# Kernel optimization log

Measured on AMD Instinct MI355X. Metric: run time of the kernel, lower is better.

The kernel has to match this reference:

```python
import jax, jax.numpy as jnp
import numpy as np

V, E, H, B, S, T = 32000, 512, 1024, 32, 64, 64

def setup_inputs() -> dict:
    key = jax.random.key(0)
    ks = jax.random.split(key, 26)
    p = 0.02  # param init scale
    inp = {
        "enc_h": jax.random.normal(ks[0], (B, S, 2 * H), dtype=jnp.float32),
        "prev_s": jax.random.normal(ks[1], (B, H), dtype=jnp.float32),
        "target": jax.random.randint(ks[2], (B, T), 0, V, dtype=jnp.int32),
        "embed": jax.random.normal(ks[3], (V, E), dtype=jnp.float32) * p,
        # Attention params
        "att_Wenc": jax.random.normal(ks[4], (2 * H, H), dtype=jnp.float32) * p,
        "att_benc": jnp.zeros((H,), dtype=jnp.float32),
        "att_Wprev": jax.random.normal(ks[5], (H, H), dtype=jnp.float32) * p,
        "att_bprev": jnp.zeros((H,), dtype=jnp.float32),
        "att_wlin": jax.random.normal(ks[6], (H, 1), dtype=jnp.float32) * p,
        "att_blin": jnp.zeros((1,), dtype=jnp.float32),
        # DecoderCell gate params (input/hidden/ctx -> 2H)
        "dc_Wi": jax.random.normal(ks[7], (E, 2 * H), dtype=jnp.float32) * p,
        "dc_bi": jnp.zeros((2 * H,), dtype=jnp.float32),
        "dc_Wh": jax.random.normal(ks[8], (H, 2 * H), dtype=jnp.float32) * p,
        "dc_bh": jnp.zeros((2 * H,), dtype=jnp.float32),
        "dc_Wc": jax.random.normal(ks[9], (2 * H, 2 * H), dtype=jnp.float32) * p,
        "dc_bc": jnp.zeros((2 * H,), dtype=jnp.float32),
        # DecoderCell candidate params (-> H)
        "dc_Wi2": jax.random.normal(ks[10], (E, H), dtype=jnp.float32) * p,
        "dc_bi2": jnp.zeros((H,), dtype=jnp.float32),
        "dc_Wh2": jax.random.normal(ks[11], (H, H), dtype=jnp.float32) * p,
        "dc_bh2": jnp.zeros((H,), dtype=jnp.float32),
        "dc_Wc2": jax.random.normal(ks[12], (2 * H, H), dtype=jnp.float32) * p,
        "dc_bc2": jnp.zeros((H,), dtype=jnp.float32),
        # dec2word
        "out_W": jax.random.normal(ks[13], (H, V), dtype=jnp.float32) * p,
        "out_b": jnp.zeros((V,), dtype=jnp.float32),
    }
    return inp


def reference(enc_h, prev_s, target, embed, att_Wenc, att_benc, att_Wprev,
              att_bprev, att_wlin, att_blin, dc_Wi, dc_bi, dc_Wh, dc_bh,
              dc_Wc, dc_bc, dc_Wi2, dc_bi2, dc_Wh2, dc_bh2, dc_Wc2, dc_bc2,
              out_W, out_b):
    h = prev_s.shape[-1]
    # Precompute attention key projection (weights fixed across timesteps)
    enc_proj = enc_h @ att_Wenc + att_benc          # B x S x H
    xs = jnp.transpose(embed[target], (1, 0, 2))    # T x B x E

    def step(s_prev, x_t):
        # Bahdanau attention
        q = s_prev @ att_Wprev + att_bprev                       # B x H
        score = jnp.tanh(enc_proj + q[:, None, :]) @ att_wlin + att_blin  # B x S x 1
        alpha = jax.nn.softmax(score[..., 0], axis=1)            # B x S (over seq)
        ctx = jnp.einsum('bs,bsh->bh', alpha, enc_h)             # B x 2H
        # GRU-like cell (original uses only the first chunk of gates)
        gates = (x_t @ dc_Wi + dc_bi) + (s_prev @ dc_Wh + dc_bh) + (ctx @ dc_Wc + dc_bc)
        reset = jax.nn.sigmoid(gates[:, :h])
        s_tilde = jnp.tanh((x_t @ dc_Wi2 + dc_bi2) + (s_prev @ dc_Wh2 + dc_bh2) + (ctx @ dc_Wc2 + dc_bc2))
        s_new = (1.0 - reset) * s_prev + reset * s_tilde
        return s_new, s_new

    final_s, dec_h = jax.lax.scan(step, prev_s, xs)   # dec_h: T x B x H
    outputs = jnp.transpose(dec_h, (1, 0, 2)) @ out_W + out_b  # B x T x V
    return outputs, final_s
```

## Files before the change

kernel.cpp:

```cpp
#include <hip/hip_runtime.h>

#define B_   32
#define S_   64
#define T_   64
#define H_   1024
#define H2_  2048
#define E_   512
#define V_   32000
#define K3_  3072
#define BT_  2048

typedef unsigned short u16;
typedef __attribute__((ext_vector_type(8))) short short8_t;
typedef __attribute__((ext_vector_type(4))) float f32x4;

__device__ __forceinline__ u16 f2bf(float f) {
  unsigned x = __float_as_uint(f);
  unsigned r = (x + 0x7fffu + ((x >> 16) & 1u)) >> 16;
  return (u16)r;
}
__device__ __forceinline__ float bf2f(u16 h) {
  return __uint_as_float(((unsigned)h) << 16);
}
__device__ __forceinline__ float frcp(float x) { return __builtin_amdgcn_rcpf(x); }
__device__ __forceinline__ float ftanh(float x) {
  float e = __expf(2.f * x);
  return 1.f - 2.f * frcp(e + 1.f);
}
__device__ __forceinline__ float fsigm(float x) {
  return frcp(1.f + __expf(-x));
}

#define KEEPV(x) asm volatile("" : "+v"(x))

__device__ __forceinline__ void st_u16(u16* p, u16 v) {
  __hip_atomic_store(p, v, __ATOMIC_RELAXED, __HIP_MEMORY_SCOPE_AGENT);
}
__device__ __forceinline__ void st_f32(float* p, float v) {
  __hip_atomic_store(p, v, __ATOMIC_RELAXED, __HIP_MEMORY_SCOPE_AGENT);
}

#define MB_ (1ull << 20)
#define KB_ (1ull << 10)
#define X_OFF    (0)
#define XGR_OFF  (4*MB_)
#define XG2_OFF  (12*MB_)
#define ENCT_OFF (20*MB_)
#define QFV_OFF  (20*MB_)
#define WQF_OFF  (28*MB_)
#define WGF_OFF  (30*MB_)
#define XSV_OFF  (28*MB_)
#define XCV_OFF  (36*MB_)
#define WOT_OFF  (0)
#define DECH_OFF (54*MB_)
#define XS0_OFF  (58*MB_)
#define BAS_OFF  (58*MB_ + 128*KB_)
#define BCR_OFF  (58*MB_ + 132*KB_)
#define BC2_OFF  (58*MB_ + 136*KB_)
#define WLB_OFF  (58*MB_ + 140*KB_)
#define BAR_OFF  (58*MB_ + 144*KB_)

__device__ __forceinline__ u16* xs_hi(char* w, int t) {
  return (u16*)(t == 0 ? (w + XS0_OFF) : (w + XSV_OFF + (size_t)(t - 1) * 131072));
}
__device__ __forceinline__ u16* xc_hi(char* w, int t) {
  return (u16*)(w + XCV_OFF + (size_t)t * 262144);
}
__device__ __forceinline__ float* qf_v(char* w, int t) {
  return (float*)(w + QFV_OFF + (size_t)t * 131072);
}


__global__ void k_gather(float* __restrict__ x, const float* __restrict__ embed,
                         const int* __restrict__ tgt) {
  int bid = blockIdx.x;
  int t = bid >> 5, b = bid & 31;
  int row = tgt[b * T_ + t];
  const float4* src = (const float4*)(embed + (size_t)row * E_);
  float4* dst = (float4*)(x + (size_t)bid * E_);
  dst[threadIdx.x] = src[threadIdx.x];
}

__global__ void k_biascomb(float* bcr, float* bc2o, float* bas, u16* wlb,
                           const float* bi, const float* bh, const float* bc,
                           const float* bi2, const float* bh2, const float* bc2i,
                           const float* benc, const float* bprev, const float* wlin) {
  int j = blockIdx.x * 256 + threadIdx.x;
  if (j < H_) {
    bcr[j]  = bi[j]  + bh[j]  + bc[j];
    bc2o[j] = bi2[j] + bh2[j] + bc2i[j];
    bas[j]  = benc[j] + bprev[j];
    wlb[j]  = f2bf(wlin[j]);
  }
}

__global__ __launch_bounds__(256) void k_gemm(
    const float* __restrict__ A, int lda,
    const float* __restrict__ Bm, int ldb,
    void* __restrict__ Cv, int ldc, int outBf16,
    const float* __restrict__ bias,
    int mtiles, int ntiles, int K) {
  __shared__ u16 As[128][72];
  __shared__ u16 Bs[128][72];
  int nwg = mtiles * ntiles;
  int bid = blockIdx.x;
  int cpx = nwg >> 3;
  int lb = (bid & 7) * cpx + (bid >> 3);
  int ntb = lb / mtiles, mtb = lb - ntb * mtiles;
  size_t m0 = (size_t)mtb * 128, n0 = (size_t)ntb * 128;
  int t = threadIdx.x, lane = t & 63, wid = t >> 6;
  int wr = (wid >> 1) * 64, wc = (wid & 1) * 64;
  f32x4 acc[4][4] = {};
  for (int k0 = 0; k0 < K; k0 += 64) {
    #pragma unroll
    for (int i = 0; i < 8; ++i) {
      int f4 = i * 256 + t;
      int row = f4 >> 4, c4 = (f4 & 15) << 2;
      float4 v = *(const float4*)(A + (m0 + row) * (size_t)lda + k0 + c4);
      ushort4 u; u.x = f2bf(v.x); u.y = f2bf(v.y); u.z = f2bf(v.z); u.w = f2bf(v.w);
      *(ushort4*)&As[row][c4] = u;
    }
    #pragma unroll
    for (int i = 0; i < 8; ++i) {
      int f4 = i * 256 + t;
      int kr = f4 >> 5, c4 = (f4 & 31) << 2;
      float4 v = *(const float4*)(Bm + (size_t)(k0 + kr) * ldb + n0 + c4);
      Bs[c4 + 0][kr] = f2bf(v.x);
      Bs[c4 + 1][kr] = f2bf(v.y);
      Bs[c4 + 2][kr] = f2bf(v.z);
      Bs[c4 + 3][kr] = f2bf(v.w);
    }
    __syncthreads();
    #pragma unroll
    for (int kk = 0; kk < 64; kk += 32) {
      int ko = kk + (lane >> 4) * 8;
      short8_t am[4], bn[4];
      #pragma unroll
      for (int m = 0; m < 4; ++m) am[m] = *(const short8_t*)&As[wr + m * 16 + (lane & 15)][ko];
      #pragma unroll
      for (int n = 0; n < 4; ++n) bn[n] = *(const short8_t*)&Bs[wc + n * 16 + (lane & 15)][ko];
      #pragma unroll
      for (int m = 0; m < 4; ++m)
        #pragma unroll
        for (int n = 0; n < 4; ++n)
          acc[m][n] = __builtin_amdgcn_mfma_f32_16x16x32_bf16(am[m], bn[n], acc[m][n], 0, 0, 0);
    }
    __syncthreads();
  }
  #pragma unroll
  for (int n = 0; n < 4; ++n) {
    int col = wc + n * 16 + (lane & 15);
    float bv = bias ? bias[n0 + col] : 0.f;
    #pragma unroll
    for (int m = 0; m < 4; ++m) {
      size_t row = m0 + wr + m * 16 + ((lane >> 4) << 2);
      #pragma unroll
      for (int r = 0; r < 4; ++r) {
        float val = acc[m][n][r] + bv;
        if (outBf16) ((u16*)Cv)[(row + r) * (size_t)ldc + n0 + col] = f2bf(val);
        else ((float*)Cv)[(row + r) * (size_t)ldc + n0 + col] = val;
      }
    }
  }
}

__global__ __launch_bounds__(256) void k_transE(u16* __restrict__ encT,
                                                const float* __restrict__ enc_h) {
  __shared__ u16 ld[64][68];
  int b = blockIdx.x >> 5, et = blockIdx.x & 31;
  int e0 = et * 64;
  int t = threadIdx.x;
  #pragma unroll
  for (int i = 0; i < 4; ++i) {
    int f4 = i * 256 + t;
    int si = f4 >> 4, e4 = (f4 & 15) << 2;
    float4 v = *(const float4*)(enc_h + ((size_t)(b * 64 + si)) * H2_ + e0 + e4);
    ld[si][e4 + 0] = f2bf(v.x); ld[si][e4 + 1] = f2bf(v.y);
    ld[si][e4 + 2] = f2bf(v.z); ld[si][e4 + 3] = f2bf(v.w);
  }
  __syncthreads();
  #pragma unroll
  for (int i = 0; i < 2; ++i) {
    int idx = i * 256 + t;
    int e = idx >> 3, s8 = (idx & 7) << 3;
    short8_t o;
    #pragma unroll
    for (int k = 0; k < 8; ++k) o[k] = (short)ld[s8 + k][e];
    *(short8_t*)(encT + ((size_t)(e0 + e)) * 2048 + b * 64 + s8) = o;
  }
}

__global__ __launch_bounds__(256) void k_packq(u16* __restrict__ wqf,
                                               const float* __restrict__ W) {
  __shared__ float ld[64][33];
  int jt = blockIdx.x & 31, kt = blockIdx.x >> 5;
  int c0 = jt * 32, k0 = kt * 64;
  int t = threadIdx.x;
  #pragma unroll
  for (int i = 0; i < 8; ++i) {
    int idx = i * 256 + t; int kr = idx >> 5, jc = idx & 31;
    ld[kr][jc] = W[(size_t)(k0 + kr) * H_ + c0 + jc];
  }
  __syncthreads();
  int u = t;
  int gl = u >> 7, kbl = (u >> 6) & 1, sub = (u >> 4) & 3, c = u & 15;
  int colLoc = gl * 16 + c;
  int gG = jt * 2 + gl, KB = kt * 2 + kbl;
  size_t lin = ((size_t)(gG * 32 + KB) * 4 + sub) * 16 + c;
  short8_t o;
  #pragma unroll
  for (int j = 0; j < 8; ++j) o[j] = (short)f2bf(ld[kbl * 32 + sub * 8 + j][colLoc]);
  *(short8_t*)(wqf + lin * 8) = o;
}

__global__ __launch_bounds__(256) void k_packg(
    u16* __restrict__ wgf, const float* __restrict__ Wh, const float* __restrict__ Wc,
    const float* __restrict__ Wh2, const float* __restrict__ Wc2) {
  __shared__ float ld[64][33];
  int sel = blockIdx.x & 1;
  int jt  = (blockIdx.x >> 1) & 31;
  int kt  = blockIdx.x >> 6;
  int k0 = kt * 64, j0 = jt * 32;
  int t = threadIdx.x;
  const float* srcW = (k0 < H_) ? (sel ? Wh2 : Wh) : (sel ? Wc2 : Wc);
  int ldw = sel ? H_ : H2_;
  int koff = (k0 < H_) ? k0 : (k0 - H_);
  #pragma unroll
  for (int i = 0; i < 8; ++i) {
    int idx = i * 256 + t; int kr = idx >> 5, jc = idx & 31;
    ld[kr][jc] = srcW[(size_t)(koff + kr) * ldw + j0 + jc];
  }
  __syncthreads();
  #pragma unroll
  for (int it = 0; it < 2; ++it) {
    int u = it * 256 + t;
    int m = u & 3, sub = (u >> 2) & 3, kbl = (u >> 4) & 1, islo = (u >> 5) & 1, gg = u >> 6;
    int jjLoc = gg * 4 + m;
    int p = 2 * (j0 + jjLoc) + sel;
    int g = p >> 3, cc = p & 7;
    int c = cc + 8 * islo;
    int KB = kt * 2 + kbl;
    size_t lin = ((size_t)(g * 96 + KB) * 4 + sub) * 16 + c;
    short8_t o;
    #pragma unroll
    for (int j = 0; j < 8; ++j) {
      float v = ld[kbl * 32 + sub * 8 + j][jjLoc];
      u16 h = f2bf(v);
      o[j] = (short)(islo ? f2bf(v - bf2f(h)) : h);
    }
    *(short8_t*)(wgf + lin * 8) = o;
  }
}

__global__ __launch_bounds__(256) void k_wtrans(u16* __restrict__ wot,
                                                const float* __restrict__ W, int nbase) {
  __shared__ u16 ld[64][68];
  int nt = blockIdx.x % 250, kt = blockIdx.x / 250;
  int n0 = nbase + nt * 64, k0 = kt * 64;
  int t = threadIdx.x;
  #pragma unroll
  for (int i = 0; i < 4; ++i) {
    int f4 = i * 256 + t;
    int kr = f4 >> 4, n4 = (f4 & 15) << 2;
    float4 v = *(const float4*)(W + (size_t)(k0 + kr) * V_ + n0 + n4);
    ld[kr][n4 + 0] = f2bf(v.x); ld[kr][n4 + 1] = f2bf(v.y);
    ld[kr][n4 + 2] = f2bf(v.z); ld[kr][n4 + 3] = f2bf(v.w);
  }
  __syncthreads();
  #pragma unroll
  for (int i = 0; i < 2; ++i) {
    int idx = i * 256 + t;
    int n = idx >> 3, k8 = (idx & 7) << 3;
    short8_t o;
    #pragma unroll
    for (int k = 0; k < 8; ++k) o[k] = (short)ld[k8 + k][n];
    *(short8_t*)(wot + ((size_t)(nt * 64 + n)) * H_ + k0 + k8) = o;
  }
}

__global__ __launch_bounds__(256) void k_gemm2(
    const u16* __restrict__ A, const u16* __restrict__ Bt,
    float* __restrict__ C, const float* __restrict__ bias, int n0g) {
  __shared__ u16 As[128][72];
  __shared__ u16 Bs[128][72];
  int bid = blockIdx.x;
  int lb = (bid & 7) * 250 + (bid >> 3);
  int mtb = lb & 15, ntb = lb >> 4;
  size_t m0 = (size_t)mtb * 128;
  size_t nl0 = (size_t)ntb * 128;
  int t = threadIdx.x, lane = t & 63, wid = t >> 6;
  int wr = (wid >> 1) * 64, wc = (wid & 1) * 64;
  f32x4 acc[4][4] = {};
  for (int k0 = 0; k0 < H_; k0 += 64) {
    #pragma unroll
    for (int i = 0; i < 4; ++i) {
      int idx = i * 256 + t;
      int row = idx >> 3, c8 = (idx & 7) << 3;
      *(short8_t*)&As[row][c8] = *(const short8_t*)(A + (m0 + row) * H_ + k0 + c8);
      *(short8_t*)&Bs[row][c8] = *(const short8_t*)(Bt + (nl0 + row) * H_ + k0 + c8);
    }
    __syncthreads();
    #pragma unroll
    for (int kk = 0; kk < 64; kk += 32) {
      int ko = kk + (lane >> 4) * 8;
      short8_t am[4], bn[4];
      #pragma unroll
      for (int m = 0; m < 4; ++m) am[m] = *(const short8_t*)&As[wr + m * 16 + (lane & 15)][ko];
      #pragma unroll
      for (int n = 0; n < 4; ++n) bn[n] = *(const short8_t*)&Bs[wc + n * 16 + (lane & 15)][ko];
      #pragma unroll
      for (int m = 0; m < 4; ++m)
        #pragma unroll
        for (int n = 0; n < 4; ++n)
          acc[m][n] = __builtin_amdgcn_mfma_f32_16x16x32_bf16(am[m], bn[n], acc[m][n], 0, 0, 0);
    }
    __syncthreads();
  }
  #pragma unroll
  for (int n = 0; n < 4; ++n) {
    int col = n0g + (int)nl0 + wc + n * 16 + (lane & 15);
    float bv = bias[col];
    #pragma unroll
    for (int m = 0; m < 4; ++m) {
      size_t row = m0 + wr + m * 16 + ((lane >> 4) << 2);
      #pragma unroll
      for (int r = 0; r < 4; ++r)
        C[(row + r) * (size_t)V_ + col] = acc[m][n][r] + bv;
    }
  }
}


__device__ __forceinline__ void gridbar(int* bar, int target) {
  asm volatile("s_waitcnt vmcnt(0)" ::: "memory");
  __syncthreads();
  if (threadIdx.x == 0) {
    int* leafcnt = bar;
    int* root    = bar + 512;
    int* leafep  = bar + 768;
    int li = blockIdx.x >> 3;
    if (__hip_atomic_fetch_add(&leafcnt[li * 16], 1, __ATOMIC_RELAXED, __HIP_MEMORY_SCOPE_AGENT) == 7) {
      __hip_atomic_store(&leafcnt[li * 16], 0, __ATOMIC_RELAXED, __HIP_MEMORY_SCOPE_AGENT);
      if (__hip_atomic_fetch_add(root, 1, __ATOMIC_RELAXED, __HIP_MEMORY_SCOPE_AGENT) == 31) {
        __hip_atomic_store(root, 0, __ATOMIC_RELAXED, __HIP_MEMORY_SCOPE_AGENT);
        #pragma unroll
        for (int i = 0; i < 32; ++i)
          __hip_atomic_store(&leafep[i * 16], target, __ATOMIC_RELAXED, __HIP_MEMORY_SCOPE_AGENT);
      }
    }
    while (__hip_atomic_load(&leafep[li * 16], __ATOMIC_RELAXED, __HIP_MEMORY_SCOPE_AGENT) != target)
      __builtin_amdgcn_s_sleep(2);
  }
  __syncthreads();
}

#define MFMA16(a, b, c) __builtin_amdgcn_mfma_f32_16x16x32_bf16((a), (b), (c), 0, 0, 0)

__global__ __launch_bounds__(512, 1) void k_mega(
    char* w, u16* __restrict__ dech, float* __restrict__ fout,
    const u16* __restrict__ wqf, const u16* __restrict__ wgf,
    const u16* __restrict__ encp, const u16* __restrict__ encT,
    const float* __restrict__ xgr, const float* __restrict__ xg2,
    const float* __restrict__ prev_s, const u16* __restrict__ wlb,
    int* bar) {
  const int t = threadIdx.x, blk = blockIdx.x;
  const int lane = t & 63, wid = t >> 6;
  const int l15 = lane & 15, l4 = lane >> 4;
  const int klo = l4 * 8;
  __shared__ short8_t wg_lds[6144];
  __shared__ f32x4 scr[1024];
  __shared__ float sc[64];
  int ep = 0;

  for (int i = t; i < 6144; i += 512)
    wg_lds[i] = *(const short8_t*)(wgf + ((size_t)blk * 6144 + i) * 8);

  const int gq = blk & 63;
  short8_t wq[4];
  #pragma unroll
  for (int i = 0; i < 4; ++i) {
    wq[i] = *(const short8_t*)(wqf + ((size_t)(gq * 32 + wid * 4 + i) * 64 + lane) * 8);
    KEEPV(wq[i]);
  }
  const int bb = blk >> 3, eg = blk & 7;
  short8_t epv[8][2];
  #pragma unroll
  for (int r = 0; r < 8; ++r) {
    const u16* p = encp + ((size_t)(bb * 64 + wid * 8 + r)) * H_ + lane * 16;
    epv[r][0] = *(const short8_t*)(p);     KEEPV(epv[r][0]);
    epv[r][1] = *(const short8_t*)(p + 8); KEEPV(epv[r][1]);
  }
  short8_t wlv[2];
  wlv[0] = *(const short8_t*)(wlb + lane * 16);     KEEPV(wlv[0]);
  wlv[1] = *(const short8_t*)(wlb + lane * 16 + 8); KEEPV(wlv[1]);
  const int eloc = t >> 1, half = t & 1;
  const int ecol = eg * 256 + eloc;
  short8_t et[4];
  #pragma unroll
  for (int i = 0; i < 4; ++i) {
    et[i] = *(const short8_t*)(encT + (size_t)ecol * 2048 + bb * 64 + half * 32 + i * 8);
    KEEPV(et[i]);
  }

  const int pc4 = blk * 8 + l15, jcol = pc4 >> 1, isc = pc4 & 1;
  const int rb = wid * 16 + l4 * 4;
  const bool fin = (wid < 2) && (l15 < 8);
  float sreg[4] = {0.f, 0.f, 0.f, 0.f};

  {
    int idx = blk * 512 + t;
    u16* xs0h = xs_hi(w, 0);
    u16* xs0l = xs0h + B_ * H_;
    if (idx < B_ * H_) {
      float v = prev_s[idx];
      u16 h = f2bf(v);
      st_u16(&xs0h[idx], h);
      st_u16(&xs0l[idx], f2bf(v - bf2f(h)));
    }
    if (fin) {
      #pragma unroll
      for (int r = 0; r < 4; ++r) sreg[r] = prev_s[(rb + r) * H_ + jcol];
    }
  }
  gridbar(bar, ++ep);

  for (int ts = 0; ts < T_; ++ts) {
    const u16* xsh = xs_hi(w, ts);
    const u16* xsl = xsh + B_ * H_;
    u16* xch = xc_hi(w, ts);
    u16* xcl = xch + B_ * H2_;
    float* qfv = qf_v(w, ts);

    float xv[4] = {0.f, 0.f, 0.f, 0.f};
    if (fin) {
      const float* xg = isc ? xg2 : xgr;
      #pragma unroll
      for (int r = 0; r < 4; ++r)
        xv[r] = xg[((size_t)ts * B_ + rb + r) * H_ + jcol];
    }
    short8_t pA[4], pB[4];
    #pragma unroll
    for (int i = 0; i < 4; ++i) {
      int k = (wid + 8 * i) * 32 + klo;
      pA[i] = *(const short8_t*)(xsh + l15 * H_ + k);        KEEPV(pA[i]);
      pB[i] = *(const short8_t*)(xsh + (l15 + 16) * H_ + k); KEEPV(pB[i]);
    }

    if (blk < 64) {
      f32x4 aA = {}, aB = {};
      #pragma unroll
      for (int i = 0; i < 4; ++i) {
        int kof = (wid * 4 + i) * 32 + klo;
        short8_t avA = *(const short8_t*)(xsh + l15 * H_ + kof);
        short8_t avB = *(const short8_t*)(xsh + (l15 + 16) * H_ + kof);
        aA = MFMA16(avA, wq[i], aA);
        aB = MFMA16(avB, wq[i], aB);
      }
      scr[(wid * 2 + 0) * 64 + lane] = aA;
      scr[(wid * 2 + 1) * 64 + lane] = aB;
      __syncthreads();
      if (wid < 2) {
        f32x4 s = scr[wid * 64 + lane];
        #pragma unroll
        for (int i = 1; i < 8; ++i) s += scr[(i * 2 + wid) * 64 + lane];
        int col = gq * 16 + l15;
        #pragma unroll
        for (int r = 0; r < 4; ++r)
          st_f32(&qfv[(size_t)(rb + r) * H_ + col], s[r]);
      }
    }
    gridbar(bar, ++ep);

    {
      float qv[16];
      #pragma unroll
      for (int i = 0; i < 4; ++i) {
        float4 s0 = *(const float4*)(qfv + (size_t)bb * H_ + lane * 16 + i * 4);
        qv[i * 4 + 0] = s0.x; qv[i * 4 + 1] = s0.y;
        qv[i * 4 + 2] = s0.z; qv[i * 4 + 3] = s0.w;
      }
      #pragma unroll
      for (int r = 0; r < 8; ++r) {
        float p = 0.f;
        #pragma unroll
        for (int jj = 0; jj < 16; ++jj)
          p += ftanh(bf2f((u16)epv[r][jj >> 3][jj & 7]) + qv[jj]) * bf2f((u16)wlv[jj >> 3][jj & 7]);
        #pragma unroll
        for (int off = 32; off; off >>= 1) p += __shfl_xor(p, off, 64);
        if (lane == 0) sc[wid * 8 + r] = p;
      }
      __syncthreads();
      if (wid == 0) {
        float v = sc[lane];
        float m = v;
        #pragma unroll
        for (int off = 32; off; off >>= 1) m = fmaxf(m, __shfl_xor(m, off, 64));
        float e = __expf(v - m);
        float s = e;
        #pragma unroll
        for (int off = 32; off; off >>= 1) s += __shfl_xor(s, off, 64);
        sc[lane] = e * frcp(s);
      }
      __syncthreads();
      {
        float a = 0.f;
        #pragma unroll
        for (int i = 0; i < 4; ++i)
          #pragma unroll
          for (int j = 0; j < 8; ++j)
            a += sc[half * 32 + i * 8 + j] * bf2f((u16)et[i][j]);
        a += __shfl_xor(a, 1, 64);
        if (half == 0) {
          u16 hh = f2bf(a);
          st_u16(&xch[bb * H2_ + ecol], hh);
          st_u16(&xcl[bb * H2_ + ecol], f2bf(a - bf2f(hh)));
        }
      }
    }
    gridbar(bar, ++ep);

    {
      f32x4 aA = {}, aB = {};
      short8_t loA[4], loB[4];
      #pragma unroll
      for (int i = 0; i < 4; ++i) {
        int k = (wid + 8 * i) * 32 + klo;
        loA[i] = *(const short8_t*)(xsl + l15 * H_ + k);
        loB[i] = *(const short8_t*)(xsl + (l15 + 16) * H_ + k);
      }
      #pragma unroll
      for (int i = 0; i < 4; ++i) {
        short8_t bv = wg_lds[(wid + 8 * i) * 64 + lane];
        aA = MFMA16(pA[i], bv, aA);
        aB = MFMA16(pB[i], bv, aB);
      }
      #pragma unroll
      for (int i = 0; i < 4; ++i) {
        short8_t bv = wg_lds[(wid + 8 * i) * 64 + lane];
        aA = MFMA16(loA[i], bv, aA);
        aB = MFMA16(loB[i], bv, aB);
      }
      #pragma unroll
      for (int i = 4; i < 12; ++i) {
        int kb = wid + 8 * i;
        int k = kb * 32 + klo - H_;
        short8_t hA = *(const short8_t*)(xch + l15 * H2_ + k);
        short8_t lA = *(const short8_t*)(xcl + l15 * H2_ + k);
        short8_t hB = *(const short8_t*)(xch + (l15 + 16) * H2_ + k);
        short8_t lB = *(const short8_t*)(xcl + (l15 + 16) * H2_ + k);
        short8_t bv = wg_lds[kb * 64 + lane];
        aA = MFMA16(hA, bv, aA);
        aA = MFMA16(lA, bv, aA);
        aB = MFMA16(hB, bv, aB);
        aB = MFMA16(lB, bv, aB);
      }
      scr[(wid * 2 + 0) * 64 + lane] = aA;
      scr[(wid * 2 + 1) * 64 + lane] = aB;
      __syncthreads();
      if (wid < 2) {
        f32x4 s = scr[wid * 64 + lane];
        #pragma unroll
        for (int i = 1; i < 8; ++i) s += scr[(i * 2 + wid) * 64 + lane];
        float tot[4];
        #pragma unroll
        for (int r = 0; r < 4; ++r) tot[r] = s[r] + __shfl_xor(s[r], 8, 64);
        if (l15 < 8) {
          u16* nsh = xs_hi(w, ts + 1);
          u16* nsl = nsh + B_ * H_;
          #pragma unroll
          for (int r = 0; r < 4; ++r) {
            int brow = rb + r;
            float pre = tot[r] + xv[r];
            float mate = __shfl_xor(pre, 1, 64);
            float rpre = isc ? mate : pre;
            float cpre = isc ? pre : mate;
            float rg = fsigm(rpre);
            float cg = ftanh(cpre);
            float sp = sreg[r];
            float sn = sp + rg * (cg - sp);
            sreg[r] = sn;
            if (!isc) {
              u16 hh = f2bf(sn);
              st_u16(&nsh[brow * H_ + jcol], hh);
              st_u16(&nsl[brow * H_ + jcol], f2bf(sn - bf2f(hh)));
              dech[((size_t)brow * T_ + ts) * H_ + jcol] = hh;
              if (ts == T_ - 1) fout[brow * H_ + jcol] = sn;
            }
          }
        }
      }
    }
    gridbar(bar, ++ep);
  }
}


extern "C" void kernel_launch(void* const* d_in, const int* in_sizes, int n_in,
                              void* d_out, int out_size, void* d_ws, size_t ws_size,
                              hipStream_t stream) {
  const float* enc_h    = (const float*)d_in[0];
  const float* prev_s   = (const float*)d_in[1];
  const int*   target   = (const int*)d_in[2];
  const float* embed    = (const float*)d_in[3];
  const float* att_Wenc = (const float*)d_in[4];
  const float* att_benc = (const float*)d_in[5];
  const float* att_Wprev= (const float*)d_in[6];
  const float* att_bprev= (const float*)d_in[7];
  const float* att_wlin = (const float*)d_in[8];
  const float* dc_Wi    = (const float*)d_in[10];
  const float* dc_bi    = (const float*)d_in[11];
  const float* dc_Wh    = (const float*)d_in[12];
  const float* dc_bh    = (const float*)d_in[13];
  const float* dc_Wc    = (const float*)d_in[14];
  const float* dc_bc    = (const float*)d_in[15];
  const float* dc_Wi2   = (const float*)d_in[16];
  const float* dc_bi2   = (const float*)d_in[17];
  const float* dc_Wh2   = (const float*)d_in[18];
  const float* dc_bh2   = (const float*)d_in[19];
  const float* dc_Wc2   = (const float*)d_in[20];
  const float* dc_bc2   = (const float*)d_in[21];
  const float* out_W    = (const float*)d_in[22];
  const float* out_b    = (const float*)d_in[23];

  char* w = (char*)d_ws;
  float* x    = (float*)(w + X_OFF);
  float* xgr  = (float*)(w + XGR_OFF);
  float* xg2  = (float*)(w + XG2_OFF);
  u16*  encp  = (u16*)(w + X_OFF);
  u16*  encT  = (u16*)(w + ENCT_OFF);
  u16*  wqf   = (u16*)(w + WQF_OFF);
  u16*  wgf   = (u16*)(w + WGF_OFF);
  u16*  wot   = (u16*)(w + WOT_OFF);
  u16*  dech  = (u16*)(w + DECH_OFF);
  float* bas  = (float*)(w + BAS_OFF);
  float* bcr  = (float*)(w + BCR_OFF);
  float* bc2  = (float*)(w + BC2_OFF);
  u16*  wlb   = (u16*)(w + WLB_OFF);
  int*  bar   = (int*)(w + BAR_OFF);
  float* fout = (float*)d_out + (size_t)BT_ * V_;

  hipMemsetAsync(bar, 0, 8192, stream);

  k_gather  <<<BT_, 128, 0, stream>>>(x, embed, target);
  k_biascomb<<<4, 256, 0, stream>>>(bcr, bc2, bas, wlb,
                                    dc_bi, dc_bh, dc_bc, dc_bi2, dc_bh2, dc_bc2,
                                    att_benc, att_bprev, att_wlin);
  k_gemm<<<16 * 8, 256, 0, stream>>>(x, E_, dc_Wi,  H2_, xgr, H_, 0, bcr, 16, 8, E_);
  k_gemm<<<16 * 8, 256, 0, stream>>>(x, E_, dc_Wi2, H_,  xg2, H_, 0, bc2, 16, 8, E_);
  k_gemm<<<16 * 8, 256, 0, stream>>>(enc_h, H2_, att_Wenc, H_, encp, H_, 1, bas, 16, 8, H2_);
  k_transE<<<1024, 256, 0, stream>>>(encT, enc_h);
  k_packq <<<512, 256, 0, stream>>>(wqf, att_Wprev);
  k_packg <<<3072, 256, 0, stream>>>(wgf, dc_Wh, dc_Wc, dc_Wh2, dc_Wc2);

  k_mega<<<256, 512, 0, stream>>>(w, dech, fout,
                                  wqf, wgf, encp, encT, xgr, xg2,
                                  prev_s, wlb, bar);

  k_wtrans<<<4000, 256, 0, stream>>>(wot, out_W, 0);
  k_gemm2 <<<2000, 256, 0, stream>>>(dech, wot, (float*)d_out, out_b, 0);
  k_wtrans<<<4000, 256, 0, stream>>>(wot, out_W, 16000);
  k_gemm2 <<<2000, 256, 0, stream>>>(dech, wot, (float*)d_out, out_b, 16000);
}
```

Before: 3.188 ms.

## Replace grid barrier for attention query with per-batch local sync and merge prep kernels

Each block of the persistent decoder kernel now computes its own slice of the query projection redundantly from a repacked Wprev. It writes partial attention scores and synchronises only with the 8 blocks sharing a batch row through a counter, instead of a full grid barrier after a 64-block query GEMM. The many small preprocessing kernels (gather, transpose, weight packing, enc projection GEMM, bias combine) are fused into one launch, and the two input GEMMs into another, to cut launch overhead. The workspace layout is rearranged to fit the new buffers. The cost is redundant scalar (non-MFMA) query work per block and extra partial-score traffic.

```diff
diff --git a/kernel.cpp b/kernel.cpp
--- a/kernel.cpp
+++ b/kernel.cpp
@@ -43,22 +43,23 @@
 #define MB_ (1ull << 20)
 #define KB_ (1ull << 10)
 #define X_OFF    (0)
+#define SPP_OFF  (0)
 #define XGR_OFF  (4*MB_)
 #define XG2_OFF  (12*MB_)
 #define ENCT_OFF (20*MB_)
-#define QFV_OFF  (20*MB_)
-#define WQF_OFF  (28*MB_)
-#define WGF_OFF  (30*MB_)
-#define XSV_OFF  (28*MB_)
-#define XCV_OFF  (36*MB_)
+#define XCV_OFF  (20*MB_)
+#define ENCP_OFF (28*MB_)
+#define W2_OFF   (36*MB_)
+#define WGF_OFF  (38*MB_)
+#define XSV_OFF  (38*MB_)
+#define DECH_OFF (46*MB_)
 #define WOT_OFF  (0)
-#define DECH_OFF (54*MB_)
-#define XS0_OFF  (58*MB_)
-#define BAS_OFF  (58*MB_ + 128*KB_)
-#define BCR_OFF  (58*MB_ + 132*KB_)
-#define BC2_OFF  (58*MB_ + 136*KB_)
-#define WLB_OFF  (58*MB_ + 140*KB_)
-#define BAR_OFF  (58*MB_ + 144*KB_)
+#define XS0_OFF  (62*MB_)
+#define MB_OFF   (62*MB_ + 128*KB_)
+#define BAR_OFF  (62*MB_ + 256*KB_)
+#define WLB_OFF  (62*MB_ + 272*KB_)
+#define BCR_OFF  (62*MB_ + 276*KB_)
+#define BC2_OFF  (62*MB_ + 280*KB_)
 
 __device__ __forceinline__ u16* xs_hi(char* w, int t) {
   return (u16*)(t == 0 ? (w + XS0_OFF) : (w + XSV_OFF + (size_t)(t - 1) * 131072));
@@ -66,44 +67,19 @@
 __device__ __forceinline__ u16* xc_hi(char* w, int t) {
   return (u16*)(w + XCV_OFF + (size_t)t * 262144);
 }
-__device__ __forceinline__ float* qf_v(char* w, int t) {
-  return (float*)(w + QFV_OFF + (size_t)t * 131072);
-}
-
-
-__global__ void k_gather(float* __restrict__ x, const float* __restrict__ embed,
-                         const int* __restrict__ tgt) {
-  int bid = blockIdx.x;
-  int t = bid >> 5, b = bid & 31;
-  int row = tgt[b * T_ + t];
-  const float4* src = (const float4*)(embed + (size_t)row * E_);
-  float4* dst = (float4*)(x + (size_t)bid * E_);
-  dst[threadIdx.x] = src[threadIdx.x];
-}
-
-__global__ void k_biascomb(float* bcr, float* bc2o, float* bas, u16* wlb,
-                           const float* bi, const float* bh, const float* bc,
-                           const float* bi2, const float* bh2, const float* bc2i,
-                           const float* benc, const float* bprev, const float* wlin) {
-  int j = blockIdx.x * 256 + threadIdx.x;
-  if (j < H_) {
-    bcr[j]  = bi[j]  + bh[j]  + bc[j];
-    bc2o[j] = bi2[j] + bh2[j] + bc2i[j];
-    bas[j]  = benc[j] + bprev[j];
-    wlb[j]  = f2bf(wlin[j]);
-  }
-}
-
-__global__ __launch_bounds__(256) void k_gemm(
-    const float* __restrict__ A, int lda,
-    const float* __restrict__ Bm, int ldb,
-    void* __restrict__ Cv, int ldc, int outBf16,
-    const float* __restrict__ bias,
-    int mtiles, int ntiles, int K) {
-  __shared__ u16 As[128][72];
-  __shared__ u16 Bs[128][72];
+__device__ __forceinline__ float* spp_v(char* w, int t) {
+  return (float*)(w + SPP_OFF + (size_t)t * 65536);
+}
+
+__device__ void gemm_body(char* smemRaw,
+                          const float* __restrict__ A, int lda,
+                          const float* __restrict__ Bm, int ldb,
+                          void* __restrict__ Cv, int ldc, int outBf16,
+                          const float* __restrict__ bias, const float* __restrict__ bias2,
+                          int mtiles, int ntiles, int K, int bid) {
+  u16 (*As)[72] = (u16(*)[72])smemRaw;
+  u16 (*Bs)[72] = (u16(*)[72])(smemRaw + 128 * 72 * 2);
   int nwg = mtiles * ntiles;
-  int bid = blockIdx.x;
   int cpx = nwg >> 3;
   int lb = (bid & 7) * cpx + (bid >> 3);
   int ntb = lb / mtiles, mtb = lb - ntb * mtiles;
@@ -151,6 +127,7 @@
   for (int n = 0; n < 4; ++n) {
     int col = wc + n * 16 + (lane & 15);
     float bv = bias ? bias[n0 + col] : 0.f;
+    if (bias2) bv += bias2[n0 + col];
     #pragma unroll
     for (int m = 0; m < 4; ++m) {
       size_t row = m0 + wr + m * 16 + ((lane >> 4) << 2);
@@ -164,92 +141,127 @@
   }
 }
 
-__global__ __launch_bounds__(256) void k_transE(u16* __restrict__ encT,
-                                                const float* __restrict__ enc_h) {
-  __shared__ u16 ld[64][68];
-  int b = blockIdx.x >> 5, et = blockIdx.x & 31;
-  int e0 = et * 64;
-  int t = threadIdx.x;
-  #pragma unroll
-  for (int i = 0; i < 4; ++i) {
-    int f4 = i * 256 + t;
-    int si = f4 >> 4, e4 = (f4 & 15) << 2;
-    float4 v = *(const float4*)(enc_h + ((size_t)(b * 64 + si)) * H2_ + e0 + e4);
-    ld[si][e4 + 0] = f2bf(v.x); ld[si][e4 + 1] = f2bf(v.y);
-    ld[si][e4 + 2] = f2bf(v.z); ld[si][e4 + 3] = f2bf(v.w);
-  }
-  __syncthreads();
-  #pragma unroll
-  for (int i = 0; i < 2; ++i) {
-    int idx = i * 256 + t;
-    int e = idx >> 3, s8 = (idx & 7) << 3;
+__global__ __launch_bounds__(256) void k_prep(
+    float* __restrict__ x, const float* __restrict__ embed, const int* __restrict__ tgt,
+    u16* __restrict__ encT, const float* __restrict__ enc_h,
+    u16* __restrict__ w2, const float* __restrict__ Wprev,
+    u16* __restrict__ wgf, const float* __restrict__ Wh, const float* __restrict__ Wc,
+    const float* __restrict__ Wh2, const float* __restrict__ Wc2,
+    u16* __restrict__ encp, const float* __restrict__ Wenc,
+    const float* __restrict__ benc, const float* __restrict__ bprev,
+    float* __restrict__ bcr, float* __restrict__ bc2o, u16* __restrict__ wlb,
+    const float* __restrict__ bi, const float* __restrict__ bh, const float* __restrict__ bc,
+    const float* __restrict__ bi2, const float* __restrict__ bh2, const float* __restrict__ bc2i,
+    const float* __restrict__ wlin) {
+  __shared__ char pbuf[36864];
+  const int bid = blockIdx.x, t = threadIdx.x;
+
+  if (bid < 1024) {
+    int f4id = bid * 256 + t;
+    int row = f4id >> 7, c4 = f4id & 127;
+    int tt = row >> 5, bbb = row & 31;
+    int trow = tgt[bbb * T_ + tt];
+    ((float4*)x)[(size_t)row * 128 + c4] = ((const float4*)embed)[(size_t)trow * 128 + c4];
+  } else if (bid < 2048) {
+    u16 (*ld)[68] = (u16(*)[68])pbuf;
+    int teb = bid - 1024;
+    int b = teb >> 5, et = teb & 31;
+    int e0 = et * 64;
+    #pragma unroll
+    for (int i = 0; i < 4; ++i) {
+      int f4 = i * 256 + t;
+      int si = f4 >> 4, e4 = (f4 & 15) << 2;
+      float4 v = *(const float4*)(enc_h + ((size_t)(b * 64 + si)) * H2_ + e0 + e4);
+      ld[si][e4 + 0] = f2bf(v.x); ld[si][e4 + 1] = f2bf(v.y);
+      ld[si][e4 + 2] = f2bf(v.z); ld[si][e4 + 3] = f2bf(v.w);
+    }
+    __syncthreads();
+    #pragma unroll
+    for (int i = 0; i < 2; ++i) {
+      int idx = i * 256 + t;
+      int e = idx >> 3, s8 = (idx & 7) << 3;
+      short8_t o;
+      #pragma unroll
+      for (int k = 0; k < 8; ++k) o[k] = (short)ld[s8 + k][e];
+      *(short8_t*)(encT + ((size_t)(e0 + e)) * 2048 + b * 64 + s8) = o;
+    }
+  } else if (bid < 2560) {
+    float (*ld)[33] = (float(*)[33])pbuf;
+    int pb = bid - 2048;
+    int kt = pb >> 5, jt = pb & 31;
+    int k0 = kt * 64, j0 = jt * 32;
+    #pragma unroll
+    for (int i = 0; i < 8; ++i) {
+      int idx = i * 256 + t; int kr = idx >> 5, jc = idx & 31;
+      ld[kr][jc] = Wprev[(size_t)(k0 + kr) * H_ + j0 + jc];
+    }
+    __syncthreads();
+    int jloc = t >> 3, kk8 = t & 7;
+    int j = j0 + jloc;
+    int eg = j >> 7;
+    int th = ((j & 127) << 2) | (kt >> 2);
+    int i = ((kt & 3) << 3) | kk8;
     short8_t o;
     #pragma unroll
-    for (int k = 0; k < 8; ++k) o[k] = (short)ld[s8 + k][e];
-    *(short8_t*)(encT + ((size_t)(e0 + e)) * 2048 + b * 64 + s8) = o;
-  }
-}
-
-__global__ __launch_bounds__(256) void k_packq(u16* __restrict__ wqf,
-                                               const float* __restrict__ W) {
-  __shared__ float ld[64][33];
-  int jt = blockIdx.x & 31, kt = blockIdx.x >> 5;
-  int c0 = jt * 32, k0 = kt * 64;
-  int t = threadIdx.x;
-  #pragma unroll
-  for (int i = 0; i < 8; ++i) {
-    int idx = i * 256 + t; int kr = idx >> 5, jc = idx & 31;
-    ld[kr][jc] = W[(size_t)(k0 + kr) * H_ + c0 + jc];
-  }
-  __syncthreads();
-  int u = t;
-  int gl = u >> 7, kbl = (u >> 6) & 1, sub = (u >> 4) & 3, c = u & 15;
-  int colLoc = gl * 16 + c;
-  int gG = jt * 2 + gl, KB = kt * 2 + kbl;
-  size_t lin = ((size_t)(gG * 32 + KB) * 4 + sub) * 16 + c;
-  short8_t o;
-  #pragma unroll
-  for (int j = 0; j < 8; ++j) o[j] = (short)f2bf(ld[kbl * 32 + sub * 8 + j][colLoc]);
-  *(short8_t*)(wqf + lin * 8) = o;
-}
-
-__global__ __launch_bounds__(256) void k_packg(
-    u16* __restrict__ wgf, const float* __restrict__ Wh, const float* __restrict__ Wc,
-    const float* __restrict__ Wh2, const float* __restrict__ Wc2) {
-  __shared__ float ld[64][33];
-  int sel = blockIdx.x & 1;
-  int jt  = (blockIdx.x >> 1) & 31;
-  int kt  = blockIdx.x >> 6;
-  int k0 = kt * 64, j0 = jt * 32;
-  int t = threadIdx.x;
-  const float* srcW = (k0 < H_) ? (sel ? Wh2 : Wh) : (sel ? Wc2 : Wc);
-  int ldw = sel ? H_ : H2_;
-  int koff = (k0 < H_) ? k0 : (k0 - H_);
-  #pragma unroll
-  for (int i = 0; i < 8; ++i) {
-    int idx = i * 256 + t; int kr = idx >> 5, jc = idx & 31;
-    ld[kr][jc] = srcW[(size_t)(koff + kr) * ldw + j0 + jc];
-  }
-  __syncthreads();
-  #pragma unroll
-  for (int it = 0; it < 2; ++it) {
-    int u = it * 256 + t;
-    int m = u & 3, sub = (u >> 2) & 3, kbl = (u >> 4) & 1, islo = (u >> 5) & 1, gg = u >> 6;
-    int jjLoc = gg * 4 + m;
-    int p = 2 * (j0 + jjLoc) + sel;
-    int g = p >> 3, cc = p & 7;
-    int c = cc + 8 * islo;
-    int KB = kt * 2 + kbl;
-    size_t lin = ((size_t)(g * 96 + KB) * 4 + sub) * 16 + c;
-    short8_t o;
-    #pragma unroll
-    for (int j = 0; j < 8; ++j) {
-      float v = ld[kbl * 32 + sub * 8 + j][jjLoc];
-      u16 h = f2bf(v);
-      o[j] = (short)(islo ? f2bf(v - bf2f(h)) : h);
-    }
-    *(short8_t*)(wgf + lin * 8) = o;
-  }
+    for (int e = 0; e < 8; ++e) o[e] = (short)f2bf(ld[kk8 * 8 + e][jloc]);
+    *(short8_t*)(w2 + ((size_t)((eg * 512 + th) * 32 + i)) * 8) = o;
+  } else if (bid < 5632) {
+    float (*ld)[33] = (float(*)[33])pbuf;
+    int pgb = bid - 2560;
+    int sel = pgb & 1;
+    int jt  = (pgb >> 1) & 31;
+    int kt  = pgb >> 6;
+    int k0 = kt * 64, j0 = jt * 32;
+    const float* srcW = (k0 < H_) ? (sel ? Wh2 : Wh) : (sel ? Wc2 : Wc);
+    int ldw = sel ? H_ : H2_;
+    int koff = (k0 < H_) ? k0 : (k0 - H_);
+    #pragma unroll
+    for (int i = 0; i < 8; ++i) {
+      int idx = i * 256 + t; int kr = idx >> 5, jc = idx & 31;
+      ld[kr][jc] = srcW[(size_t)(koff + kr) * ldw + j0 + jc];
+    }
+    __syncthreads();
+    #pragma unroll
+    for (int it = 0; it < 2; ++it) {
+      int u = it * 256 + t;
+      int m = u & 3, sub = (u >> 2) & 3, kbl = (u >> 4) & 1, islo = (u >> 5) & 1, gg = u >> 6;
+      int jjLoc = gg * 4 + m;
+      int p = 2 * (j0 + jjLoc) + sel;
+      int g = p >> 3, cc = p & 7;
+      int c = cc + 8 * islo;
+      int KB = kt * 2 + kbl;
+      size_t lin = ((size_t)(g * 96 + KB) * 4 + sub) * 16 + c;
+      short8_t o;
+      #pragma unroll
+      for (int j = 0; j < 8; ++j) {
+        float v = ld[kbl * 32 + sub * 8 + j][jjLoc];
+        u16 h = f2bf(v);
+        o[j] = (short)(islo ? f2bf(v - bf2f(h)) : h);
+      }
+      *(short8_t*)(wgf + lin * 8) = o;
+    }
+  } else if (bid < 5760) {
+    gemm_body(pbuf, enc_h, H2_, Wenc, H_, encp, H_, 1, benc, bprev, 16, 8, H2_, bid - 5632);
+  } else {
+    int j = (bid - 5760) * 256 + t;
+    if (j < H_) {
+      bcr[j]  = bi[j]  + bh[j]  + bc[j];
+      bc2o[j] = bi2[j] + bh2[j] + bc2i[j];
+      wlb[j]  = f2bf(wlin[j]);
+    }
+  }
+}
+
+__global__ __launch_bounds__(256) void k_gemm12(
+    const float* __restrict__ x,
+    const float* __restrict__ Wi, const float* __restrict__ Wi2,
+    float* __restrict__ xgr, float* __restrict__ xg2,
+    const float* __restrict__ bcr, const float* __restrict__ bc2) {
+  __shared__ char pbuf[36864];
+  if (blockIdx.x < 128)
+    gemm_body(pbuf, x, E_, Wi, H2_, xgr, H_, 0, bcr, nullptr, 16, 8, E_, blockIdx.x);
+  else
+    gemm_body(pbuf, x, E_, Wi2, H_, xg2, H_, 0, bc2, nullptr, 16, 8, E_, blockIdx.x - 128);
 }
 
 __global__ __launch_bounds__(256) void k_wtrans(u16* __restrict__ wot,
@@ -358,11 +370,11 @@
 
 __global__ __launch_bounds__(512, 1) void k_mega(
     char* w, u16* __restrict__ dech, float* __restrict__ fout,
-    const u16* __restrict__ wqf, const u16* __restrict__ wgf,
+    const u16* __restrict__ w2, const u16* __restrict__ wgf,
     const u16* __restrict__ encp, const u16* __restrict__ encT,
     const float* __restrict__ xgr, const float* __restrict__ xg2,
     const float* __restrict__ prev_s, const u16* __restrict__ wlb,
-    int* bar) {
+    int* bar, int* mb) {
   const int t = threadIdx.x, blk = blockIdx.x;
   const int lane = t & 63, wid = t >> 6;
   const int l15 = lane & 15, l4 = lane >> 4;
@@ -370,29 +382,25 @@
   __shared__ short8_t wg_lds[6144];
   __shared__ f32x4 scr[1024];
   __shared__ float sc[64];
+  __shared__ u16 sL[1024];
+  __shared__ float qL[128];
   int ep = 0;
 
   for (int i = t; i < 6144; i += 512)
     wg_lds[i] = *(const short8_t*)(wgf + ((size_t)blk * 6144 + i) * 8);
 
-  const int gq = blk & 63;
-  short8_t wq[4];
-  #pragma unroll
-  for (int i = 0; i < 4; ++i) {
-    wq[i] = *(const short8_t*)(wqf + ((size_t)(gq * 32 + wid * 4 + i) * 64 + lane) * 8);
-    KEEPV(wq[i]);
-  }
   const int bb = blk >> 3, eg = blk & 7;
-  short8_t epv[8][2];
-  #pragma unroll
-  for (int r = 0; r < 8; ++r) {
-    const u16* p = encp + ((size_t)(bb * 64 + wid * 8 + r)) * H_ + lane * 16;
-    epv[r][0] = *(const short8_t*)(p);     KEEPV(epv[r][0]);
-    epv[r][1] = *(const short8_t*)(p + 8); KEEPV(epv[r][1]);
-  }
-  short8_t wlv[2];
-  wlv[0] = *(const short8_t*)(wlb + lane * 16);     KEEPV(wlv[0]);
-  wlv[1] = *(const short8_t*)(wlb + lane * 16 + 8); KEEPV(wlv[1]);
+
+  const int si_a = t >> 3, jg = t & 7;
+  short8_t epv2[2], wlv2[2];
+  {
+    const u16* p = encp + ((size_t)(bb * 64 + si_a)) * H_ + eg * 128 + jg * 16;
+    epv2[0] = *(const short8_t*)(p);     KEEPV(epv2[0]);
+    epv2[1] = *(const short8_t*)(p + 8); KEEPV(epv2[1]);
+    const u16* q = wlb + eg * 128 + jg * 16;
+    wlv2[0] = *(const short8_t*)(q);     KEEPV(wlv2[0]);
+    wlv2[1] = *(const short8_t*)(q + 8); KEEPV(wlv2[1]);
+  }
   const int eloc = t >> 1, half = t & 1;
   const int ecol = eg * 256 + eloc;
   short8_t et[4];
@@ -429,7 +437,8 @@
     const u16* xsl = xsh + B_ * H_;
     u16* xch = xc_hi(w, ts);
     u16* xcl = xch + B_ * H2_;
-    float* qfv = qf_v(w, ts);
+    float* spp = spp_v(w, ts);
+    int* mbp = mb + (ts * 32 + bb) * 16;
 
     float xv[4] = {0.f, 0.f, 0.f, 0.f};
     if (fin) {
@@ -446,75 +455,74 @@
       pB[i] = *(const short8_t*)(xsh + (l15 + 16) * H_ + k); KEEPV(pB[i]);
     }
 
-    if (blk < 64) {
-      f32x4 aA = {}, aB = {};
-      #pragma unroll
-      for (int i = 0; i < 4; ++i) {
-        int kof = (wid * 4 + i) * 32 + klo;
-        short8_t avA = *(const short8_t*)(xsh + l15 * H_ + kof);
-        short8_t avB = *(const short8_t*)(xsh + (l15 + 16) * H_ + kof);
-        aA = MFMA16(avA, wq[i], aA);
-        aB = MFMA16(avB, wq[i], aB);
-      }
-      scr[(wid * 2 + 0) * 64 + lane] = aA;
-      scr[(wid * 2 + 1) * 64 + lane] = aB;
-      __syncthreads();
-      if (wid < 2) {
-        f32x4 s = scr[wid * 64 + lane];
+    if (t < 128)
+      *(short8_t*)&sL[t * 8] = *(const short8_t*)(xsh + bb * H_ + t * 8);
+    __syncthreads();
+    {
+      float qa = 0.f;
+      const u16* wp = w2 + ((size_t)(eg * 512 + t)) * 256;
+      const u16* sp = sL + (t & 3) * 256;
+      #pragma unroll
+      for (int i = 0; i < 32; ++i) {
+        short8_t wv = *(const short8_t*)(wp + i * 8);
+        short8_t sv = *(const short8_t*)(sp + i * 8);
         #pragma unroll
-        for (int i = 1; i < 8; ++i) s += scr[(i * 2 + wid) * 64 + lane];
-        int col = gq * 16 + l15;
+        for (int e = 0; e < 8; ++e)
+          qa += bf2f((u16)wv[e]) * bf2f((u16)sv[e]);
+      }
+      qa += __shfl_xor(qa, 1, 64);
+      qa += __shfl_xor(qa, 2, 64);
+      if ((t & 3) == 0) qL[t >> 2] = qa;
+    }
+    __syncthreads();
+    {
+      float p = 0.f;
+      #pragma unroll
+      for (int jj = 0; jj < 16; ++jj) {
+        float qv = qL[jg * 16 + jj];
+        p += ftanh(bf2f((u16)epv2[jj >> 3][jj & 7]) + qv) * bf2f((u16)wlv2[jj >> 3][jj & 7]);
+      }
+      p += __shfl_xor(p, 1, 64);
+      p += __shfl_xor(p, 2, 64);
+      p += __shfl_xor(p, 4, 64);
+      if (jg == 0) st_f32(&spp[(bb * 64 + si_a) * 8 + eg], p);
+    }
+    asm volatile("s_waitcnt vmcnt(0)" ::: "memory");
+    __syncthreads();
+    if (t == 0) {
+      __hip_atomic_fetch_add(mbp, 1, __ATOMIC_RELAXED, __HIP_MEMORY_SCOPE_AGENT);
+      while (__hip_atomic_load(mbp, __ATOMIC_RELAXED, __HIP_MEMORY_SCOPE_AGENT) != 8)
+        __builtin_amdgcn_s_sleep(1);
+    }
+    __syncthreads();
+
+    if (wid == 0) {
+      const float* pp = spp + ((size_t)(bb * 64 + lane)) * 8;
+      float4 a0 = *(const float4*)(pp);
+      float4 a1 = *(const float4*)(pp + 4);
+      float v = (a0.x + a0.y + a0.z + a0.w) + (a1.x + a1.y + a1.z + a1.w);
+      float m = v;
+      #pragma unroll
+      for (int off = 32; off; off >>= 1) m = fmaxf(m, __shfl_xor(m, off, 64));
+      float e = __expf(v - m);
+      float s = e;
+      #pragma unroll
+      for (int off = 32; off; off >>= 1) s += __shfl_xor(s, off, 64);
+      sc[lane] = e * frcp(s);
+    }
+    __syncthreads();
+    {
+      float a = 0.f;
+      #pragma unroll
+      for (int i = 0; i < 4; ++i)
         #pragma unroll
-        for (int r = 0; r < 4; ++r)
-          st_f32(&qfv[(size_t)(rb + r) * H_ + col], s[r]);
-      }
-    }
-    gridbar(bar, ++ep);
-
-    {
-      float qv[16];
-      #pragma unroll
-      for (int i = 0; i < 4; ++i) {
-        float4 s0 = *(const float4*)(qfv + (size_t)bb * H_ + lane * 16 + i * 4);
-        qv[i * 4 + 0] = s0.x; qv[i * 4 + 1] = s0.y;
-        qv[i * 4 + 2] = s0.z; qv[i * 4 + 3] = s0.w;
-      }
-      #pragma unroll
-      for (int r = 0; r < 8; ++r) {
-        float p = 0.f;
-        #pragma unroll
-        for (int jj = 0; jj < 16; ++jj)
-          p += ftanh(bf2f((u16)epv[r][jj >> 3][jj & 7]) + qv[jj]) * bf2f((u16)wlv[jj >> 3][jj & 7]);
-        #pragma unroll
-        for (int off = 32; off; off >>= 1) p += __shfl_xor(p, off, 64);
-        if (lane == 0) sc[wid * 8 + r] = p;
-      }
-      __syncthreads();
-      if (wid == 0) {
-        float v = sc[lane];
-        float m = v;
-        #pragma unroll
-        for (int off = 32; off; off >>= 1) m = fmaxf(m, __shfl_xor(m, off, 64));
-        float e = __expf(v - m);
-        float s = e;
-        #pragma unroll
-        for (int off = 32; off; off >>= 1) s += __shfl_xor(s, off, 64);
-        sc[lane] = e * frcp(s);
-      }
-      __syncthreads();
-      {
-        float a = 0.f;
-        #pragma unroll
-        for (int i = 0; i < 4; ++i)
-          #pragma unroll
-          for (int j = 0; j < 8; ++j)
-            a += sc[half * 32 + i * 8 + j] * bf2f((u16)et[i][j]);
-        a += __shfl_xor(a, 1, 64);
-        if (half == 0) {
-          u16 hh = f2bf(a);
-          st_u16(&xch[bb * H2_ + ecol], hh);
-          st_u16(&xcl[bb * H2_ + ecol], f2bf(a - bf2f(hh)));
-        }
+        for (int j = 0; j < 8; ++j)
+          a += sc[half * 32 + i * 8 + j] * bf2f((u16)et[i][j]);
+      a += __shfl_xor(a, 1, 64);
+      if (half == 0) {
+        u16 hh = f2bf(a);
+        st_u16(&xch[bb * H2_ + ecol], hh);
+        st_u16(&xcl[bb * H2_ + ecol], f2bf(a - bf2f(hh)));
       }
     }
     gridbar(bar, ++ep);
@@ -626,35 +634,31 @@
   float* x    = (float*)(w + X_OFF);
   float* xgr  = (float*)(w + XGR_OFF);
   float* xg2  = (float*)(w + XG2_OFF);
-  u16*  encp  = (u16*)(w + X_OFF);
   u16*  encT  = (u16*)(w + ENCT_OFF);
-  u16*  wqf   = (u16*)(w + WQF_OFF);
+  u16*  encp  = (u16*)(w + ENCP_OFF);
+  u16*  w2    = (u16*)(w + W2_OFF);
   u16*  wgf   = (u16*)(w + WGF_OFF);
   u16*  wot   = (u16*)(w + WOT_OFF);
   u16*  dech  = (u16*)(w + DECH_OFF);
-  float* bas  = (float*)(w + BAS_OFF);
+  u16*  wlb   = (u16*)(w + WLB_OFF);
   float* bcr  = (float*)(w + BCR_OFF);
   float* bc2  = (float*)(w + BC2_OFF);
-  u16*  wlb   = (u16*)(w + WLB_OFF);
   int*  bar   = (int*)(w + BAR_OFF);
+  int*  mb    = (int*)(w + MB_OFF);
   float* fout = (float*)d_out + (size_t)BT_ * V_;
 
-  hipMemsetAsync(bar, 0, 8192, stream);
-
-  k_gather  <<<BT_, 128, 0, stream>>>(x, embed, target);
-  k_biascomb<<<4, 256, 0, stream>>>(bcr, bc2, bas, wlb,
-                                    dc_bi, dc_bh, dc_bc, dc_bi2, dc_bh2, dc_bc2,
-                                    att_benc, att_bprev, att_wlin);
-  k_gemm<<<16 * 8, 256, 0, stream>>>(x, E_, dc_Wi,  H2_, xgr, H_, 0, bcr, 16, 8, E_);
-  k_gemm<<<16 * 8, 256, 0, stream>>>(x, E_, dc_Wi2, H_,  xg2, H_, 0, bc2, 16, 8, E_);
-  k_gemm<<<16 * 8, 256, 0, stream>>>(enc_h, H2_, att_Wenc, H_, encp, H_, 1, bas, 16, 8, H2_);
-  k_transE<<<1024, 256, 0, stream>>>(encT, enc_h);
-  k_packq <<<512, 256, 0, stream>>>(wqf, att_Wprev);
-  k_packg <<<3072, 256, 0, stream>>>(wgf, dc_Wh, dc_Wc, dc_Wh2, dc_Wc2);
+  hipMemsetAsync(w + MB_OFF, 0, 136 * KB_, stream);
+
+  k_prep<<<5764, 256, 0, stream>>>(x, embed, target, encT, enc_h,
+                                   w2, att_Wprev, wgf, dc_Wh, dc_Wc, dc_Wh2, dc_Wc2,
+                                   encp, att_Wenc, att_benc, att_bprev,
+                                   bcr, bc2, wlb,
+                                   dc_bi, dc_bh, dc_bc, dc_bi2, dc_bh2, dc_bc2, att_wlin);
+  k_gemm12<<<256, 256, 0, stream>>>(x, dc_Wi, dc_Wi2, xgr, xg2, bcr, bc2);
 
   k_mega<<<256, 512, 0, stream>>>(w, dech, fout,
-                                  wqf, wgf, encp, encT, xgr, xg2,
-                                  prev_s, wlb, bar);
+                                  w2, wgf, encp, encT, xgr, xg2,
+                                  prev_s, wlb, bar, mb);
 
   k_wtrans<<<4000, 256, 0, stream>>>(wot, out_W, 0);
   k_gemm2 <<<2000, 256, 0, stream>>>(dech, wot, (float*)d_out, out_b, 0);
```

After: 2.781 ms. 12.8% less time.
